# Kernel tuning notes

Hardware: AMD Instinct MI355X
Metric: run time of the kernel (lower is better)

## Reference

```python
import jax, jax.numpy as jnp
import numpy as np

B, L, D, H = 4, 4096, 1024, 16
Dh = D // H
DECAY_INIT, DECAY_RANGE = 5.0, 1.0
LN_EPS = 1e-5


def setup_inputs() -> dict:
    key = jax.random.key(0)
    ks = jax.random.split(key, 5)
    s = 1.0 / np.sqrt(D)
    x = jax.random.normal(ks[0], (B, L, D), dtype=jnp.float32)
    Wq = jax.random.normal(ks[1], (D, D), dtype=jnp.float32) * s
    Wv = jax.random.normal(ks[2], (D, D), dtype=jnp.float32) * s
    Wo = jax.random.normal(ks[3], (D, D), dtype=jnp.float32) * s
    Wg = jax.random.normal(ks[4], (D, D), dtype=jnp.float32) * s
    # per-head decay logits, matching __init__: 5.0 + 1.0 * h / H
    beta = DECAY_INIT + DECAY_RANGE * (jnp.arange(H, dtype=jnp.float32) / H)
    ln_gamma = jnp.ones((D,), dtype=jnp.float32)
    ln_beta = jnp.zeros((D,), dtype=jnp.float32)
    return {"x": x, "Wq": Wq, "Wv": Wv, "Wo": Wo, "Wg": Wg,
            "beta": beta, "ln_gamma": ln_gamma, "ln_beta": ln_beta}


def _retention_scan(v, lam):
    # v: (B,L,H,Dh), lam: (H,); s_t = lam * s_{t-1} + v_t  (s_{-1} = 0)
    a = jnp.broadcast_to(lam[None, None, :, None], v.shape)

    def combine(c1, c2):
        a1, b1 = c1
        a2, b2 = c2
        return a1 * a2, a2 * b1 + b2

    _, s = jax.lax.associative_scan(combine, (a, v), axis=1)
    return s


def _layernorm(x, gamma, beta):
    mu = jnp.mean(x, axis=-1, keepdims=True)
    var = jnp.mean(jnp.square(x - mu), axis=-1, keepdims=True)
    return (x - mu) * jax.lax.rsqrt(var + LN_EPS) * gamma + beta


def reference(x, Wq, Wv, Wo, Wg, beta, ln_gamma, ln_beta):
    b, l, d = x.shape
    # decay lambda per head: (1 - 2^-beta) clamped to (tiny, 1 - 1e-9)
    tiny = jnp.finfo(jnp.float32).tiny
    lam = jnp.clip(1.0 - jnp.exp2(-beta), tiny, 1.0 - 1e-9)
    q = (x @ Wq.T).reshape(b, l, H, Dh)
    v = (x @ Wv.T).reshape(b, l, H, Dh)
    state = _retention_scan(v, lam)             # (B,L,H,Dh)
    ret = (q * state).reshape(b, l, d)          # per-timestep retention readout
    y = _layernorm(ret, ln_gamma, ln_beta)
    g = jax.nn.silu(x @ Wg.T)                   # swish gate
    out = (y * g) @ Wo.T
    return out
```

## Files before the change

### kernel.cpp

```cpp
#include <hip/hip_runtime.h>
#include <hip/hip_bf16.h>
#include <cfloat>

#define BB 4
#define LL 4096
#define DD 1024
#define HH 16
#define DHH 64
#define MM (BB * LL)
#define LN_EPS 1e-5f
#define LDQVG 3072
#define SCC 16
#define NCHUNK (LL / SCC)

typedef __hip_bfloat16 bf16;
typedef __attribute__((ext_vector_type(8))) short short8;
typedef __attribute__((ext_vector_type(4))) float float4_t;

struct bf16x4 { bf16 a, b, c, d; };
struct alignas(16) bf8 { bf16 e[8]; };

__device__ __forceinline__ float b2f(bf16 u) {
    union { unsigned int i; float f; } c;
    c.i = ((unsigned int)__bfloat16_as_ushort(u)) << 16;
    return c.f;
}

__device__ __forceinline__ float lam_of(const float* beta, int head) {
    float lam = 1.0f - exp2f(-beta[head]);
    return fminf(fmaxf(lam, 1.1754944e-38f), 1.0f - 1e-9f);
}

__global__ __launch_bounds__(256) void cvt_f32_bf16(const float* __restrict__ in,
                                                    bf16* __restrict__ out, int n) {
    int i = (blockIdx.x * 256 + threadIdx.x) * 4;
    if (i >= n) return;
    float4 f = *(const float4*)(in + i);
    bf16x4 o;
    o.a = __float2bfloat16(f.x);
    o.b = __float2bfloat16(f.y);
    o.c = __float2bfloat16(f.z);
    o.d = __float2bfloat16(f.w);
    *(bf16x4*)(out + i) = o;
}

__global__ __launch_bounds__(256) void cvt4_weights(const float* __restrict__ w0,
                                                    const float* __restrict__ w1,
                                                    const float* __restrict__ w2,
                                                    const float* __restrict__ w3,
                                                    bf16* __restrict__ o) {
    int which = blockIdx.x >> 10;
    int i = ((blockIdx.x & 1023) * 256 + threadIdx.x) * 4;
    const float* w = (which == 0) ? w0 : (which == 1) ? w1 : (which == 2) ? w2 : w3;
    float4 f = *(const float4*)(w + i);
    bf16x4 r;
    r.a = __float2bfloat16(f.x);
    r.b = __float2bfloat16(f.y);
    r.c = __float2bfloat16(f.z);
    r.d = __float2bfloat16(f.w);
    *(bf16x4*)(o + (size_t)which * 1048576 + i) = r;
}

__device__ __forceinline__ void async16(const bf16* g, bf16* l) {
    __builtin_amdgcn_global_load_lds(
        (const __attribute__((address_space(1))) void*)g,
        (__attribute__((address_space(3))) void*)l,
        16, 0, 0);
}

template <typename OutT, int KK>
__global__ __launch_bounds__(256) void gemm_bt(const bf16* __restrict__ A,
                                               const bf16* __restrict__ Bm,
                                               OutT* __restrict__ C,
                                               int M, int N, int ldc) {
    __shared__ bf16 sA[128 * 32];
    __shared__ bf16 sB[128 * 32];

    const int t    = threadIdx.x;
    const int lane = t & 63;
    const int wave = t >> 6;
    const int wm   = (wave >> 1) * 64;
    const int wn   = (wave & 1) * 64;

    const int bm = blockIdx.x;
    const int bn = blockIdx.y;

    const int c1 = t, c2 = t + 256;
    const int r1 = c1 >> 2, g1 = ((c1 & 3) - (c1 >> 3)) & 3;
    const int r2 = c2 >> 2, g2 = ((c2 & 3) - (c2 >> 3)) & 3;
    const bf16* gA1 = A  + (size_t)(bm * 128 + r1) * KK + g1 * 8;
    const bf16* gA2 = A  + (size_t)(bm * 128 + r2) * KK + g2 * 8;
    const bf16* gB1 = Bm + (size_t)(bn * 128 + r1) * KK + g1 * 8;
    const bf16* gB2 = Bm + (size_t)(bn * 128 + r2) * KK + g2 * 8;
    bf16* lA1 = sA + c1 * 8;
    bf16* lA2 = sA + c2 * 8;
    bf16* lB1 = sB + c1 * 8;
    bf16* lB2 = sB + c2 * 8;

    const int kg = lane >> 4;
    const bf16* ra[4];
    const bf16* rb[4];
#pragma unroll
    for (int mi = 0; mi < 4; ++mi) {
        int r = wm + (lane & 15) + mi * 16;
        ra[mi] = sA + (r * 4 + ((kg + (r >> 1)) & 3)) * 8;
    }
#pragma unroll
    for (int ni = 0; ni < 4; ++ni) {
        int r = wn + (lane & 15) + ni * 16;
        rb[ni] = sB + (r * 4 + ((kg + (r >> 1)) & 3)) * 8;
    }

    float4_t acc[4][4] = {};

#pragma unroll 1
    for (int it = 0; it < KK / 32; ++it) {
        async16(gA1, lA1);
        async16(gA2, lA2);
        async16(gB1, lB1);
        async16(gB2, lB2);
        gA1 += 32; gA2 += 32; gB1 += 32; gB2 += 32;
        __syncthreads();

        short8 af[4], bfr[4];
#pragma unroll
        for (int mi = 0; mi < 4; ++mi) af[mi]  = *(const short8*)ra[mi];
#pragma unroll
        for (int ni = 0; ni < 4; ++ni) bfr[ni] = *(const short8*)rb[ni];

#pragma unroll
        for (int mi = 0; mi < 4; ++mi)
#pragma unroll
            for (int ni = 0; ni < 4; ++ni)
                acc[mi][ni] = __builtin_amdgcn_mfma_f32_16x16x32_bf16(
                    af[mi], bfr[ni], acc[mi][ni], 0, 0, 0);
        __syncthreads();
    }

    const int rbase = bm * 128 + wm + ((lane >> 4) << 2);
    const int cbase = bn * 128 + wn + (lane & 15);
#pragma unroll
    for (int mi = 0; mi < 4; ++mi) {
#pragma unroll
        for (int ni = 0; ni < 4; ++ni) {
#pragma unroll
            for (int r = 0; r < 4; ++r) {
                int row = rbase + mi * 16 + r;
                int col = cbase + ni * 16;
                C[(size_t)row * ldc + col] = (OutT)acc[mi][ni][r];
            }
        }
    }
}

__global__ __launch_bounds__(64) void scan_chunksum(const bf16* __restrict__ qvg,
                                                    const float* __restrict__ beta,
                                                    float* __restrict__ S) {
    const int c    = blockIdx.x;
    const int half = blockIdx.y;
    const int b    = blockIdx.z;
    const int tid  = threadIdx.x;
    const int dh0  = half * 512 + tid * 8;
    const float lam = lam_of(beta, dh0 >> 6);

    const bf16* vp = qvg + 1024 + ((size_t)(b * LL + c * SCC)) * LDQVG + dh0;

    float s[8] = {};
#pragma unroll
    for (int t = 0; t < SCC; ++t) {
        bf8 vv = *(const bf8*)(vp + (size_t)t * LDQVG);
#pragma unroll
        for (int j = 0; j < 8; ++j)
            s[j] = fmaf(s[j], lam, b2f(vv.e[j]));
    }

    float* sp = S + ((size_t)(b * NCHUNK + c)) * DD + dh0;
    float4 lo = {s[0], s[1], s[2], s[3]};
    float4 hi = {s[4], s[5], s[6], s[7]};
    *(float4*)(sp)     = lo;
    *(float4*)(sp + 4) = hi;
}

__global__ __launch_bounds__(64) void scan_carry(const float* __restrict__ S,
                                                 float* __restrict__ T,
                                                 const float* __restrict__ beta) {
    const int gid = blockIdx.x * 64 + threadIdx.x;
    const int b = gid >> 10;
    const int f = gid & 1023;
    const float lam  = lam_of(beta, f >> 6);
    const float lamC = powf(lam, (float)SCC);

    const size_t base = (size_t)b * NCHUNK * DD + f;
    float t = 0.0f;
    for (int c = 0; c < NCHUNK; ++c) {
        float s = S[base + (size_t)c * DD];
        T[base + (size_t)c * DD] = t;
        t = fmaf(t, lamC, s);
    }
}

__global__ __launch_bounds__(64) void scan_apply(bf16* __restrict__ qvg,
                                                 const float* __restrict__ beta,
                                                 const float* __restrict__ T) {
    const int c    = blockIdx.x;
    const int half = blockIdx.y;
    const int b    = blockIdx.z;
    const int tid  = threadIdx.x;
    const int dh0  = half * 512 + tid * 8;
    const float lam = lam_of(beta, dh0 >> 6);

    const float* tp = T + ((size_t)(b * NCHUNK + c)) * DD + dh0;
    float4 lo = *(const float4*)(tp);
    float4 hi = *(const float4*)(tp + 4);
    float s[8] = {lo.x, lo.y, lo.z, lo.w, hi.x, hi.y, hi.z, hi.w};

    bf16* qp = qvg + ((size_t)(b * LL + c * SCC)) * LDQVG + dh0;

#pragma unroll
    for (int t = 0; t < SCC; ++t) {
        const size_t off = (size_t)t * LDQVG;
        bf8 vv = *(const bf8*)(qp + 1024 + off);
        bf8 qq = *(const bf8*)(qp + off);
        bf8 o;
#pragma unroll
        for (int j = 0; j < 8; ++j) {
            s[j] = fmaf(s[j], lam, b2f(vv.e[j]));
            o.e[j] = __float2bfloat16(b2f(qq.e[j]) * s[j]);
        }
        *(bf8*)(qp + off) = o;
    }
}

__global__ __launch_bounds__(256) void ln_gate(const bf16* __restrict__ qvg,
                                               const float* __restrict__ gamma,
                                               const float* __restrict__ betaln,
                                               bf16* __restrict__ z) {
    const int row  = blockIdx.x;
    const int tid  = threadIdx.x;
    const int lane = tid & 63;
    const int wave = tid >> 6;
    const size_t rbase = (size_t)row * LDQVG + tid * 4;

    bf16x4 rv = *(const bf16x4*)(qvg + rbase);
    float x0 = b2f(rv.a), x1 = b2f(rv.b), x2 = b2f(rv.c), x3 = b2f(rv.d);

    float s  = x0 + x1 + x2 + x3;
    float s2 = x0 * x0 + x1 * x1 + x2 * x2 + x3 * x3;
#pragma unroll
    for (int off = 32; off >= 1; off >>= 1) {
        s  += __shfl_xor(s, off, 64);
        s2 += __shfl_xor(s2, off, 64);
    }
    __shared__ float red[8];
    if (lane == 0) { red[wave] = s; red[wave + 4] = s2; }
    __syncthreads();
    s  = red[0] + red[1] + red[2] + red[3];
    s2 = red[4] + red[5] + red[6] + red[7];

    const float mu   = s * (1.0f / DD);
    const float var  = s2 * (1.0f / DD) - mu * mu;
    const float rstd = rsqrtf(var + LN_EPS);

    bf16x4 gv = *(const bf16x4*)(qvg + rbase + 2048);
    float4 gm = *(const float4*)(gamma + tid * 4);
    float4 bt = *(const float4*)(betaln + tid * 4);

    float xs[4]  = {x0, x1, x2, x3};
    float gs[4]  = {b2f(gv.a), b2f(gv.b), b2f(gv.c), b2f(gv.d)};
    float gmm[4] = {gm.x, gm.y, gm.z, gm.w};
    float btt[4] = {bt.x, bt.y, bt.z, bt.w};

    bf16x4 o;
    bf16* op = &o.a;
#pragma unroll
    for (int j = 0; j < 4; ++j) {
        float y  = (xs[j] - mu) * rstd * gmm[j] + btt[j];
        float g  = gs[j];
        float sg = g / (1.0f + expf(-g));
        op[j] = __float2bfloat16(y * sg);
    }
    *(bf16x4*)(z + (size_t)row * DD + tid * 4) = o;
}

extern "C" void kernel_launch(void* const* d_in, const int* in_sizes, int n_in,
                              void* d_out, int out_size, void* d_ws, size_t ws_size,
                              hipStream_t stream) {
    const float* x     = (const float*)d_in[0];
    const float* Wq    = (const float*)d_in[1];
    const float* Wv    = (const float*)d_in[2];
    const float* Wo    = (const float*)d_in[3];
    const float* Wg    = (const float*)d_in[4];
    const float* beta  = (const float*)d_in[5];
    const float* ln_g  = (const float*)d_in[6];
    const float* ln_b  = (const float*)d_in[7];
    float* out = (float*)d_out;

    char* ws = (char*)d_ws;
    bf16*  xb   = (bf16*)ws;
    float* Sbuf = (float*)ws;
    float* Tbuf = (float*)(ws + (size_t)4 * 1024 * 1024);
    bf16*  wqb  = (bf16*)(ws + (size_t)32 * 1024 * 1024);
    bf16*  wob  = wqb + 3 * 1048576;
    bf16*  qvg  = (bf16*)(ws + (size_t)40 * 1024 * 1024);
    bf16*  zb   = xb;

    cvt_f32_bf16<<<dim3((MM * DD) / 1024), dim3(256), 0, stream>>>(x, xb, MM * DD);
    cvt4_weights<<<dim3(4096), dim3(256), 0, stream>>>(Wq, Wv, Wg, Wo, wqb);

    gemm_bt<bf16, DD><<<dim3(MM / 128, LDQVG / 128), dim3(256), 0, stream>>>(
        xb, wqb, qvg, MM, LDQVG, LDQVG);

    scan_chunksum<<<dim3(NCHUNK, 2, BB), dim3(64), 0, stream>>>(qvg, beta, Sbuf);
    scan_carry<<<dim3(64), dim3(64), 0, stream>>>(Sbuf, Tbuf, beta);
    scan_apply<<<dim3(NCHUNK, 2, BB), dim3(64), 0, stream>>>(qvg, beta, Tbuf);

    ln_gate<<<dim3(MM), dim3(256), 0, stream>>>(qvg, ln_g, ln_b, zb);

    gemm_bt<float, DD><<<dim3(MM / 128, DD / 128), dim3(256), 0, stream>>>(
        zb, wob, out, MM, DD, DD);
}
```

Baseline: 378.0 us.

## Switch GEMM to 32x32x16 MFMA with 64-wide K tiles

Rewrites the bf16 GEMM inner loop to use 32x32x16 MFMA instructions with a 2x2 accumulator grid per wave instead of 4x4 16x16x32 tiles. It also doubles the K-step staged in shared memory to 64, with a new 8-way XOR-style swizzle, halving the number of barriers per K. The larger MFMA shape needs fewer LDS fragment reads per flop. The cost is double the LDS per block, which may lower occupancy, and there is still no double buffering.

After: 349.8 us. -7.5%, faster.

```diff
diff --git a/kernel.cpp b/kernel.cpp
--- a/kernel.cpp
+++ b/kernel.cpp
@@ -15,7 +15,7 @@
 
 typedef __hip_bfloat16 bf16;
 typedef __attribute__((ext_vector_type(8))) short short8;
-typedef __attribute__((ext_vector_type(4))) float float4_t;
+typedef __attribute__((ext_vector_type(16))) float float16_t;
 
 struct bf16x4 { bf16 a, b, c, d; };
 struct alignas(16) bf8 { bf16 e[8]; };
@@ -73,8 +73,8 @@
                                                const bf16* __restrict__ Bm,
                                                OutT* __restrict__ C,
                                                int M, int N, int ldc) {
-    __shared__ bf16 sA[128 * 32];
-    __shared__ bf16 sB[128 * 32];
+    __shared__ bf16 sA[128 * 64];
+    __shared__ bf16 sB[128 * 64];
 
     const int t    = threadIdx.x;
     const int lane = t & 63;
@@ -85,69 +85,79 @@
     const int bm = blockIdx.x;
     const int bn = blockIdx.y;
 
-    const int c1 = t, c2 = t + 256;
-    const int r1 = c1 >> 2, g1 = ((c1 & 3) - (c1 >> 3)) & 3;
-    const int r2 = c2 >> 2, g2 = ((c2 & 3) - (c2 >> 3)) & 3;
-    const bf16* gA1 = A  + (size_t)(bm * 128 + r1) * KK + g1 * 8;
-    const bf16* gA2 = A  + (size_t)(bm * 128 + r2) * KK + g2 * 8;
-    const bf16* gB1 = Bm + (size_t)(bn * 128 + r1) * KK + g1 * 8;
-    const bf16* gB2 = Bm + (size_t)(bn * 128 + r2) * KK + g2 * 8;
-    bf16* lA1 = sA + c1 * 8;
-    bf16* lA2 = sA + c2 * 8;
-    bf16* lB1 = sB + c1 * 8;
-    bf16* lB2 = sB + c2 * 8;
-
-    const int kg = lane >> 4;
-    const bf16* ra[4];
-    const bf16* rb[4];
-#pragma unroll
-    for (int mi = 0; mi < 4; ++mi) {
-        int r = wm + (lane & 15) + mi * 16;
-        ra[mi] = sA + (r * 4 + ((kg + (r >> 1)) & 3)) * 8;
-    }
-#pragma unroll
-    for (int ni = 0; ni < 4; ++ni) {
-        int r = wn + (lane & 15) + ni * 16;
-        rb[ni] = sB + (r * 4 + ((kg + (r >> 1)) & 3)) * 8;
-    }
-
-    float4_t acc[4][4] = {};
+    const bf16* gA[4];
+    const bf16* gB[4];
+    bf16* lA[4];
+    bf16* lB[4];
+#pragma unroll
+    for (int j = 0; j < 4; ++j) {
+        int c = t + j * 256;
+        int r = c >> 3;
+        int g = ((c & 7) - (r & 7)) & 7;
+        gA[j] = A  + (size_t)(bm * 128 + r) * KK + g * 8;
+        gB[j] = Bm + (size_t)(bn * 128 + r) * KK + g * 8;
+        lA[j] = sA + c * 8;
+        lB[j] = sB + c * 8;
+    }
+
+    const int kh = lane >> 5;
+    const bf16* rdA[2][4];
+    const bf16* rdB[2][4];
+#pragma unroll
+    for (int mi = 0; mi < 2; ++mi) {
+        int r = wm + (lane & 31) + mi * 32;
+#pragma unroll
+        for (int tk = 0; tk < 4; ++tk) {
+            int kc = tk * 2 + kh;
+            rdA[mi][tk] = sA + (r * 8 + ((kc + r) & 7)) * 8;
+        }
+    }
+#pragma unroll
+    for (int ni = 0; ni < 2; ++ni) {
+        int r = wn + (lane & 31) + ni * 32;
+#pragma unroll
+        for (int tk = 0; tk < 4; ++tk) {
+            int kc = tk * 2 + kh;
+            rdB[ni][tk] = sB + (r * 8 + ((kc + r) & 7)) * 8;
+        }
+    }
+
+    float16_t acc[2][2] = {};
 
 #pragma unroll 1
-    for (int it = 0; it < KK / 32; ++it) {
-        async16(gA1, lA1);
-        async16(gA2, lA2);
-        async16(gB1, lB1);
-        async16(gB2, lB2);
-        gA1 += 32; gA2 += 32; gB1 += 32; gB2 += 32;
+    for (int it = 0; it < KK / 64; ++it) {
+#pragma unroll
+        for (int j = 0; j < 4; ++j) async16(gA[j], lA[j]);
+#pragma unroll
+        for (int j = 0; j < 4; ++j) async16(gB[j], lB[j]);
+#pragma unroll
+        for (int j = 0; j < 4; ++j) { gA[j] += 64; gB[j] += 64; }
         __syncthreads();
 
-        short8 af[4], bfr[4];
-#pragma unroll
-        for (int mi = 0; mi < 4; ++mi) af[mi]  = *(const short8*)ra[mi];
-#pragma unroll
-        for (int ni = 0; ni < 4; ++ni) bfr[ni] = *(const short8*)rb[ni];
-
-#pragma unroll
-        for (int mi = 0; mi < 4; ++mi)
-#pragma unroll
-            for (int ni = 0; ni < 4; ++ni)
-                acc[mi][ni] = __builtin_amdgcn_mfma_f32_16x16x32_bf16(
-                    af[mi], bfr[ni], acc[mi][ni], 0, 0, 0);
+#pragma unroll
+        for (int tk = 0; tk < 4; ++tk) {
+            short8 a0 = *(const short8*)rdA[0][tk];
+            short8 a1 = *(const short8*)rdA[1][tk];
+            short8 b0 = *(const short8*)rdB[0][tk];
+            short8 b1 = *(const short8*)rdB[1][tk];
+            acc[0][0] = __builtin_amdgcn_mfma_f32_32x32x16_bf16(a0, b0, acc[0][0], 0, 0, 0);
+            acc[0][1] = __builtin_amdgcn_mfma_f32_32x32x16_bf16(a0, b1, acc[0][1], 0, 0, 0);
+            acc[1][0] = __builtin_amdgcn_mfma_f32_32x32x16_bf16(a1, b0, acc[1][0], 0, 0, 0);
+            acc[1][1] = __builtin_amdgcn_mfma_f32_32x32x16_bf16(a1, b1, acc[1][1], 0, 0, 0);
+        }
         __syncthreads();
     }
 
-    const int rbase = bm * 128 + wm + ((lane >> 4) << 2);
-    const int cbase = bn * 128 + wn + (lane & 15);
-#pragma unroll
-    for (int mi = 0; mi < 4; ++mi) {
-#pragma unroll
-        for (int ni = 0; ni < 4; ++ni) {
-#pragma unroll
-            for (int r = 0; r < 4; ++r) {
-                int row = rbase + mi * 16 + r;
-                int col = cbase + ni * 16;
-                C[(size_t)row * ldc + col] = (OutT)acc[mi][ni][r];
+    const int col0 = bn * 128 + wn + (lane & 31);
+    const int row0 = bm * 128 + wm + 4 * (lane >> 5);
+#pragma unroll
+    for (int mi = 0; mi < 2; ++mi) {
+#pragma unroll
+        for (int ni = 0; ni < 2; ++ni) {
+#pragma unroll
+            for (int reg = 0; reg < 16; ++reg) {
+                int row = row0 + mi * 32 + (reg & 3) + 8 * (reg >> 2);
+                C[(size_t)row * ldc + col0 + ni * 32] = (OutT)acc[mi][ni][reg];
             }
         }
     }
```
